# Performance work log

Measured on AMD Instinct MI355X. Metric: run time of the kernel, lower is better.

Reference implementation:

```python
import jax, jax.numpy as jnp
import numpy as np

J = 1.0
B, C, L = 16, 16, 128


def _masks(L):
    ii, jj = jnp.meshgrid(jnp.arange(L), jnp.arange(L), indexing='ij')
    black = ((ii + jj) % 2 == 0)
    return black, jnp.logical_not(black)


def _nbr_sum(s):
    # periodic up/down/left/right neighbor sum, same math as the (i±1)%L gathers
    return (jnp.roll(s, 1, -2) + jnp.roll(s, -1, -2)
            + jnp.roll(s, 1, -1) + jnp.roll(s, -1, -1))


def _half_update(spins, mask, T, key):
    # Metropolis on one checkerboard color: dE = 2*J*s*sum_nbrs
    dE = 2.0 * J * spins * _nbr_sum(spins)
    u = jax.random.uniform(key, spins.shape, dtype=spins.dtype)
    accept = u < jnp.exp(-dE / T[:, None, None, None])
    return jnp.where(jnp.logical_and(accept, mask), -spins, spins)


def _one_sweep(spins, T, key, black, white):
    k1, k2 = jax.random.split(key)
    spins = _half_update(spins, black, T, k1)
    return _half_update(spins, white, T, k2)


def _energy(spins):
    # E = -J * sum over bonds (right + down neighbors once each) -> [B, C]
    return -J * jnp.sum(spins * (jnp.roll(spins, -1, -2) + jnp.roll(spins, -1, -1)), axis=(-2, -1))


def _pt_exchange(spins, T, key):
    nB = T.shape[0]
    P = nB // 2
    E = _energy(spins)                       # [B, C]
    beta = 1.0 / T
    E0, E1 = E[0:2 * P:2], E[1:2 * P:2]
    d = (beta[0:2 * P:2] - beta[1:2 * P:2])[:, None] * (E0 - E1)  # [P, C]
    u = jax.random.uniform(key, d.shape, dtype=spins.dtype)
    # accept prob min(1, exp(d)); exp(min(d,0)) is overflow-safe and equivalent
    acc = (u < jnp.exp(jnp.minimum(d, 0.0)))[:, :, None, None]
    s0, s1 = spins[0:2 * P:2], spins[1:2 * P:2]
    spins = spins.at[0:2 * P:2].set(jnp.where(acc, s1, s0))
    spins = spins.at[1:2 * P:2].set(jnp.where(acc, s0, s1))
    return spins


def _simulate(spins_init, T, n_sweeps, n_therm, decorrelate, pt_interval):
    Lx = spins_init.shape[-1]
    black, white = _masks(Lx)
    base = jax.random.key(42)

    def step_fn(spins, i):
        k = jax.random.fold_in(base, i)
        spins = _one_sweep(spins, T, k, black, white)
        spins = jax.lax.cond(i % pt_interval == 0,
                             lambda s: _pt_exchange(s, T, jax.random.fold_in(k, 123)),
                             lambda s: s, spins)
        return spins, None

    # thermalization
    spins, _ = jax.lax.scan(step_fn, spins_init, jnp.arange(n_therm))

    # production: record one sample per decorrelate sweeps
    num_samples = n_sweeps // decorrelate

    def block_fn(spins, b):
        spins, _ = jax.lax.scan(lambda s, j: step_fn(s, n_therm + b * decorrelate + j),
                                spins, jnp.arange(decorrelate))
        return spins, spins

    spins, samples = jax.lax.scan(block_fn, spins, jnp.arange(num_samples))
    # samples: [S, B, C, L, L] -> [B, C*S, L, L]
    Bn, Cn = spins.shape[0], spins.shape[1]
    return jnp.transpose(samples, (1, 0, 2, 3, 4)).reshape(Bn, num_samples * Cn, Lx, Lx)


def setup_inputs() -> dict:
    key = jax.random.key(0)
    k1, _ = jax.random.split(key)
    x = jax.random.normal(k1, (B, C, L, L), dtype=jnp.float32)
    spins_init = jnp.where(x >= 0, 1.0, -1.0).astype(jnp.float32)  # ±1 Ising spins
    T = jnp.linspace(1.0, 3.5, B).astype(jnp.float32)              # temperature ladder
    return {"spins_init": spins_init, "T": T, "n_sweeps": 10, "n_therm": 10,
            "decorrelate": 5, "pt_interval": 5}


def reference(spins_init, T, n_sweeps, n_therm, decorrelate, pt_interval):
    return _simulate(spins_init, T, n_sweeps, n_therm, decorrelate, pt_interval)
```

## Files before the change

### kernel.cpp

```cpp
#include <hip/hip_runtime.h>
#include <stdint.h>


#define LSZ   128
#define NB    16
#define NC    16
#define NSITES (NB*NC*LSZ*LSZ)

__host__ __device__ __forceinline__ void tf2x32(uint32_t k0, uint32_t k1,
                                                uint32_t x0, uint32_t x1,
                                                uint32_t& o0, uint32_t& o1) {
  uint32_t k2 = k0 ^ k1 ^ 0x1BD11BDAu;
  x0 += k0; x1 += k1;
#define TFR(r) { x0 += x1; x1 = (x1 << (r)) | (x1 >> (32 - (r))); x1 ^= x0; }
  TFR(13) TFR(15) TFR(26) TFR(6)
  x0 += k1; x1 += k2 + 1u;
  TFR(17) TFR(29) TFR(16) TFR(24)
  x0 += k2; x1 += k0 + 2u;
  TFR(13) TFR(15) TFR(26) TFR(6)
  x0 += k0; x1 += k1 + 3u;
  TFR(17) TFR(29) TFR(16) TFR(24)
  x0 += k1; x1 += k2 + 4u;
  TFR(13) TFR(15) TFR(26) TFR(6)
  x0 += k2; x1 += k0 + 5u;
#undef TFR
  o0 = x0; o1 = x1;
}

__device__ __forceinline__ float tf_uniform(uint32_t w) {
  union { uint32_t u; float f; } cvt;
  cvt.u = (w >> 9) | 0x3f800000u;
  return cvt.f - 1.0f;
}

__device__ __forceinline__ int sb(uint32_t w, int b) {
  return (int)((int32_t)(w << ((3 - b) * 8)) >> 24);
}

__global__ __launch_bounds__(512) void k_chunk(const float4* __restrict__ in4,
                                               uint32_t* __restrict__ sg,
                                               const float* __restrict__ T,
                                               int* __restrict__ slotmap,
                                               const float* __restrict__ Eprev,
                                               float* __restrict__ Ecur,
                                               float* __restrict__ out,
                                               int chunk, int start, int nsw,
                                               int sample_local, int sidx,
                                               int write_E, int store_back) {
  __shared__ __align__(16) uint32_t lat32[LSZ * LSZ / 4];
  __shared__ uint32_t kb[5][4];
  __shared__ float sh_p4, sh_p8;
  __shared__ int sh_bp;
  __shared__ int wred[8];

  const int w = blockIdx.x;
  const int t = threadIdx.x;
  const int c = w & 15;

  if (t < nsw) {
    uint32_t kk0, kk1, a, b;
    tf2x32(0u, 42u, 0u, (uint32_t)(start + t), kk0, kk1);
    tf2x32(kk0, kk1, 0u, 0u, a, b);
    kb[t][0] = a; kb[t][1] = b;
    tf2x32(kk0, kk1, 0u, 1u, a, b);
    kb[t][2] = a; kb[t][3] = b;
  }

  if (chunk == 0) {
    for (int k = 0; k < 8; ++k) {
      int idx = k * 512 + t;
      float4 v = in4[(w << 12) + idx];
      lat32[idx] = (v.x >= 0.0f ? 0x01u : 0xFFu)
                 | ((v.y >= 0.0f ? 0x01u : 0xFFu) << 8)
                 | ((v.z >= 0.0f ? 0x01u : 0xFFu) << 16)
                 | ((v.w >= 0.0f ? 0x01u : 0xFFu) << 24);
    }
  } else {
    for (int k = 0; k < 2; ++k)
      ((uint4*)lat32)[k * 512 + t] = ((const uint4*)sg)[(w << 10) + k * 512 + t];
  }

  if (t == 0) {
    int bp;
    if (chunk == 0) {
      bp = w >> 4;
    } else {
      bp = slotmap[w];
      int p = bp >> 1;
      float E0 = Eprev[(2 * p) * NC + c];
      float E1 = Eprev[(2 * p + 1) * NC + c];
      float b0 = 1.0f / T[2 * p];
      float b1 = 1.0f / T[2 * p + 1];
      float d = (b0 - b1) * (E0 - E1);
      uint32_t kk0, kk1, p0, p1, w0, w1;
      tf2x32(0u, 42u, 0u, (uint32_t)(start - 1), kk0, kk1);
      tf2x32(kk0, kk1, 0u, 123u, p0, p1);
      tf2x32(p0, p1, 0u, (uint32_t)(p * NC + c), w0, w1);
      float u = tf_uniform(w0 ^ w1);
      float pa = (d < 0.0f) ? (float)exp((double)d) : 1.0f;
      if (u < pa) bp ^= 1;
    }
    slotmap[w] = bp;
    sh_bp = bp;
    float Tb = T[bp];
    sh_p4 = (float)exp((double)(-4.0f / Tb));
    sh_p8 = (float)exp((double)(-8.0f / Tb));
  }
  __syncthreads();

  const int bp = sh_bp;
  const float p4 = sh_p4, p8 = sh_p8;
  const int r    = t >> 2;
  const int sg32 = t & 3;
  const int col0 = sg32 << 5;
  const uint32_t rowbase = ((uint32_t)((bp << 4) | c) << 14) + ((uint32_t)r << 7);
  const int8_t* latb = (const int8_t*)lat32;
  const int own4 = (r << 3) + (sg32 << 1);

  for (int sw = 0; sw < nsw; ++sw) {
    for (int par = 0; par < 2; ++par) {
      const uint32_t kk0 = kb[sw][par * 2];
      const uint32_t kk1 = kb[sw][par * 2 + 1];
      const int j0 = (r + par) & 1;

      uint32_t cw[8], uw[8], dw[8];
      {
        uint4 a  = ((const uint4*)lat32)[own4];
        uint4 b2 = ((const uint4*)lat32)[own4 + 1];
        cw[0]=a.x; cw[1]=a.y; cw[2]=a.z; cw[3]=a.w;
        cw[4]=b2.x; cw[5]=b2.y; cw[6]=b2.z; cw[7]=b2.w;
        int u4 = (((r - 1) & 127) << 3) + (sg32 << 1);
        a  = ((const uint4*)lat32)[u4];
        b2 = ((const uint4*)lat32)[u4 + 1];
        uw[0]=a.x; uw[1]=a.y; uw[2]=a.z; uw[3]=a.w;
        uw[4]=b2.x; uw[5]=b2.y; uw[6]=b2.z; uw[7]=b2.w;
        int d4 = (((r + 1) & 127) << 3) + (sg32 << 1);
        a  = ((const uint4*)lat32)[d4];
        b2 = ((const uint4*)lat32)[d4 + 1];
        dw[0]=a.x; dw[1]=a.y; dw[2]=a.z; dw[3]=a.w;
        dw[4]=b2.x; dw[5]=b2.y; dw[6]=b2.z; dw[7]=b2.w;
      }
      int lfb = latb[(r << 7) + ((col0 - 1) & 127)];
      int rtb = latb[(r << 7) + ((col0 + 32) & 127)];

      uint32_t ex[9];
      ex[0] = (cw[0] << 8) | (uint32_t)(uint8_t)lfb;
#pragma unroll
      for (int i = 1; i < 8; ++i) ex[i] = (cw[i - 1] >> 24) | (cw[i] << 8);
      ex[8] = (cw[7] >> 24) | ((uint32_t)(uint8_t)rtb << 8);
      uint32_t Y[9], U[8], D[8];
#pragma unroll
      for (int i = 0; i < 8; ++i) {
        Y[i] = j0 ? ((ex[i] >> 8) | (ex[i + 1] << 24)) : ex[i];
        U[i] = j0 ? ((uw[i] >> 8) | ((i < 7 ? uw[i + 1] : 0u) << 24)) : uw[i];
        D[i] = j0 ? ((dw[i] >> 8) | ((i < 7 ? dw[i + 1] : 0u) << 24)) : dw[i];
      }
      Y[8] = j0 ? (ex[8] >> 8) : ex[8];

      const uint32_t mbase = 0xFEu << (8 * j0);
      uint32_t xm[8];
#pragma unroll
      for (int i = 0; i < 8; ++i) xm[i] = 0u;
      const uint32_t cnt0 = rowbase + (uint32_t)(col0 + j0);
#pragma unroll
      for (int m = 0; m < 16; ++m) {
        int lf = sb(Y[(2 * m) >> 2], (2 * m) & 3);
        int s0 = sb(Y[(2 * m + 1) >> 2], (2 * m + 1) & 3);
        int rt = sb(Y[(2 * m + 2) >> 2], (2 * m + 2) & 3);
        int up = sb(U[(2 * m) >> 2], (2 * m) & 3);
        int dn = sb(D[(2 * m) >> 2], (2 * m) & 3);
        int q = s0 * (lf + rt + up + dn);
        uint32_t o0, o1;
        tf2x32(kk0, kk1, 0u, cnt0 + 2u * (uint32_t)m, o0, o1);
        float u = tf_uniform(o0 ^ o1);
        bool a = (q <= 0) || (u < (q == 4 ? p8 : p4));
        if (a) xm[m >> 1] |= (m & 1) ? (mbase << 16) : mbase;
      }
      uint4 n0, n1;
      n0.x = cw[0] ^ xm[0]; n0.y = cw[1] ^ xm[1];
      n0.z = cw[2] ^ xm[2]; n0.w = cw[3] ^ xm[3];
      n1.x = cw[4] ^ xm[4]; n1.y = cw[5] ^ xm[5];
      n1.z = cw[6] ^ xm[6]; n1.w = cw[7] ^ xm[7];
      ((uint4*)lat32)[own4]     = n0;
      ((uint4*)lat32)[own4 + 1] = n1;
      __syncthreads();
    }

    if (sw == sample_local) {
      float4* dst = (float4*)out
                  + (((size_t)((bp << 5) + (sidx << 4) + c)) << 12)
                  + (r << 5) + (sg32 << 3);
      const uint32_t* own = lat32 + (r << 5) + (sg32 << 3);
#pragma unroll
      for (int qd = 0; qd < 8; ++qd) {
        uint32_t v = own[qd];
        float4 f;
        f.x = (float)sb(v, 0); f.y = (float)sb(v, 1);
        f.z = (float)sb(v, 2); f.w = (float)sb(v, 3);
        dst[qd] = f;
      }
    }
  }

  if (write_E) {
    uint32_t cw[8], dw[8];
    {
      uint4 a  = ((const uint4*)lat32)[own4];
      uint4 b2 = ((const uint4*)lat32)[own4 + 1];
      cw[0]=a.x; cw[1]=a.y; cw[2]=a.z; cw[3]=a.w;
      cw[4]=b2.x; cw[5]=b2.y; cw[6]=b2.z; cw[7]=b2.w;
      int d4 = (((r + 1) & 127) << 3) + (sg32 << 1);
      a  = ((const uint4*)lat32)[d4];
      b2 = ((const uint4*)lat32)[d4 + 1];
      dw[0]=a.x; dw[1]=a.y; dw[2]=a.z; dw[3]=a.w;
      dw[4]=b2.x; dw[5]=b2.y; dw[6]=b2.z; dw[7]=b2.w;
    }
    int rb = latb[(r << 7) + ((col0 + 32) & 127)];
    int psum = 0;
#pragma unroll
    for (int i = 0; i < 32; ++i) {
      int ci = sb(cw[i >> 2], i & 3);
      int di = sb(dw[i >> 2], i & 3);
      int ri = (i < 31) ? sb(cw[(i + 1) >> 2], (i + 1) & 3) : rb;
      psum += ci * (di + ri);
    }
#pragma unroll
    for (int o = 32; o > 0; o >>= 1) psum += __shfl_down(psum, o, 64);
    if ((t & 63) == 0) wred[t >> 6] = psum;
    __syncthreads();
    if (t == 0) {
      int tot = 0;
#pragma unroll
      for (int i = 0; i < 8; ++i) tot += wred[i];
      Ecur[(bp << 4) | c] = -(float)tot;
    }
  }

  if (store_back) {
    for (int k = 0; k < 2; ++k)
      ((uint4*)sg)[(w << 10) + k * 512 + t] = ((const uint4*)lat32)[k * 512 + t];
  }
}

extern "C" void kernel_launch(void* const* d_in, const int* in_sizes, int n_in,
                              void* d_out, int out_size, void* d_ws, size_t ws_size,
                              hipStream_t stream) {
  const float* spins_in = (const float*)d_in[0];
  const float* T        = (const float*)d_in[1];
  uint32_t* s   = (uint32_t*)d_ws;
  float*  Ea    = (float*)((char*)d_ws + (4u << 20));
  float*  Eb    = (float*)((char*)d_ws + (4u << 20) + 1024);
  int*  slotmap = (int*)((char*)d_ws + (4u << 20) + 2048);
  float*  out = (float*)d_out;

  const int starts[5]  = {0, 1, 6, 11, 16};
  const int counts[5]  = {1, 5, 5, 5, 4};
  const int samploc[5] = {-1, -1, -1, 3, 3};
  const int sampidx[5] = {0, 0, 0, 0, 1};
  const int writeE[5]  = {1, 1, 1, 1, 0};
  const int storeB[5]  = {1, 1, 1, 1, 0};

  for (int ch = 0; ch < 5; ++ch) {
    float* Ecur  = (ch & 1) ? Eb : Ea;
    float* Eprev = (ch & 1) ? Ea : Eb;
    k_chunk<<<256, 512, 0, stream>>>((const float4*)spins_in, s, T, slotmap,
                                     Eprev, Ecur, out,
                                     ch, starts[ch], counts[ch],
                                     samploc[ch], sampidx[ch],
                                     writeE[ch], storeB[ch]);
  }
}
```

Baseline: 290.6 us.

## Double threads per lattice, pair Threefry streams, and use integer acceptance thresholds

Each 128x128 lattice block now runs 1024 threads instead of 512, so each thread handles 16 columns instead of 32. With 256 blocks on a device with 256 CUs, this doubles the per-CU parallelism that hides latency in the RNG-heavy Metropolis loop. Two Threefry evaluations are interleaved in one function to raise ILP, and the float uniform compare is replaced by comparing the top 23 random bits against precomputed integer thresholds. The risks are higher register pressure under 1024-thread launch bounds, and a possible off-by-rounding mismatch between the ceil-based threshold and the float compare.

```diff
diff --git a/kernel.cpp b/kernel.cpp
--- a/kernel.cpp
+++ b/kernel.cpp
@@ -27,6 +27,31 @@
   o0 = x0; o1 = x1;
 }
 
+__device__ __forceinline__ void tf2x32x2(uint32_t k0, uint32_t k1,
+                                         uint32_t xa, uint32_t xb,
+                                         uint32_t& oa, uint32_t& ob) {
+  uint32_t k2 = k0 ^ k1 ^ 0x1BD11BDAu;
+  uint32_t a0 = k0, a1 = xa + k1;
+  uint32_t b0 = k0, b1 = xb + k1;
+#define TFR2(r) { a0 += a1; b0 += b1; \
+                  a1 = __builtin_rotateleft32(a1, r); \
+                  b1 = __builtin_rotateleft32(b1, r); \
+                  a1 ^= a0; b1 ^= b0; }
+  TFR2(13) TFR2(15) TFR2(26) TFR2(6)
+  a0 += k1; a1 += k2 + 1u; b0 += k1; b1 += k2 + 1u;
+  TFR2(17) TFR2(29) TFR2(16) TFR2(24)
+  a0 += k2; a1 += k0 + 2u; b0 += k2; b1 += k0 + 2u;
+  TFR2(13) TFR2(15) TFR2(26) TFR2(6)
+  a0 += k0; a1 += k1 + 3u; b0 += k0; b1 += k1 + 3u;
+  TFR2(17) TFR2(29) TFR2(16) TFR2(24)
+  a0 += k1; a1 += k2 + 4u; b0 += k1; b1 += k2 + 4u;
+  TFR2(13) TFR2(15) TFR2(26) TFR2(6)
+  a0 += k2; a1 += k0 + 5u; b0 += k2; b1 += k0 + 5u;
+#undef TFR2
+  oa = a0 ^ a1;
+  ob = b0 ^ b1;
+}
+
 __device__ __forceinline__ float tf_uniform(uint32_t w) {
   union { uint32_t u; float f; } cvt;
   cvt.u = (w >> 9) | 0x3f800000u;
@@ -37,21 +62,21 @@
   return (int)((int32_t)(w << ((3 - b) * 8)) >> 24);
 }
 
-__global__ __launch_bounds__(512) void k_chunk(const float4* __restrict__ in4,
-                                               uint32_t* __restrict__ sg,
-                                               const float* __restrict__ T,
-                                               int* __restrict__ slotmap,
-                                               const float* __restrict__ Eprev,
-                                               float* __restrict__ Ecur,
-                                               float* __restrict__ out,
-                                               int chunk, int start, int nsw,
-                                               int sample_local, int sidx,
-                                               int write_E, int store_back) {
+__global__ __launch_bounds__(1024) void k_chunk(const float4* __restrict__ in4,
+                                                uint32_t* __restrict__ sg,
+                                                const float* __restrict__ T,
+                                                int* __restrict__ slotmap,
+                                                const float* __restrict__ Eprev,
+                                                float* __restrict__ Ecur,
+                                                float* __restrict__ out,
+                                                int chunk, int start, int nsw,
+                                                int sample_local, int sidx,
+                                                int write_E, int store_back) {
   __shared__ __align__(16) uint32_t lat32[LSZ * LSZ / 4];
   __shared__ uint32_t kb[5][4];
-  __shared__ float sh_p4, sh_p8;
+  __shared__ uint32_t sh_T4, sh_T8;
   __shared__ int sh_bp;
-  __shared__ int wred[8];
+  __shared__ int wred[16];
 
   const int w = blockIdx.x;
   const int t = threadIdx.x;
@@ -67,8 +92,8 @@
   }
 
   if (chunk == 0) {
-    for (int k = 0; k < 8; ++k) {
-      int idx = k * 512 + t;
+    for (int k = 0; k < 4; ++k) {
+      int idx = k * 1024 + t;
       float4 v = in4[(w << 12) + idx];
       lat32[idx] = (v.x >= 0.0f ? 0x01u : 0xFFu)
                  | ((v.y >= 0.0f ? 0x01u : 0xFFu) << 8)
@@ -76,8 +101,7 @@
                  | ((v.w >= 0.0f ? 0x01u : 0xFFu) << 24);
     }
   } else {
-    for (int k = 0; k < 2; ++k)
-      ((uint4*)lat32)[k * 512 + t] = ((const uint4*)sg)[(w << 10) + k * 512 + t];
+    ((uint4*)lat32)[t] = ((const uint4*)sg)[(w << 10) + t];
   }
 
   if (t == 0) {
@@ -103,19 +127,22 @@
     slotmap[w] = bp;
     sh_bp = bp;
     float Tb = T[bp];
-    sh_p4 = (float)exp((double)(-4.0f / Tb));
-    sh_p8 = (float)exp((double)(-8.0f / Tb));
+    float p4 = (float)exp((double)(-4.0f / Tb));
+    float p8 = (float)exp((double)(-8.0f / Tb));
+    sh_T4 = (uint32_t)ceil((double)p4 * 8388608.0);
+    sh_T8 = (uint32_t)ceil((double)p8 * 8388608.0);
   }
   __syncthreads();
 
   const int bp = sh_bp;
-  const float p4 = sh_p4, p8 = sh_p8;
-  const int r    = t >> 2;
-  const int sg32 = t & 3;
-  const int col0 = sg32 << 5;
+  const uint32_t T4 = sh_T4, T8 = sh_T8;
+  const uint32_t TOPEN = 0x00800000u;
+  const int r    = t >> 3;
+  const int seg  = t & 7;
+  const int col0 = seg << 4;
   const uint32_t rowbase = ((uint32_t)((bp << 4) | c) << 14) + ((uint32_t)r << 7);
   const int8_t* latb = (const int8_t*)lat32;
-  const int own4 = (r << 3) + (sg32 << 1);
+  const int own4 = (r << 3) + seg;
 
   for (int sw = 0; sw < nsw; ++sw) {
     for (int par = 0; par < 2; ++par) {
@@ -123,105 +150,95 @@
       const uint32_t kk1 = kb[sw][par * 2 + 1];
       const int j0 = (r + par) & 1;
 
-      uint32_t cw[8], uw[8], dw[8];
-      {
-        uint4 a  = ((const uint4*)lat32)[own4];
-        uint4 b2 = ((const uint4*)lat32)[own4 + 1];
-        cw[0]=a.x; cw[1]=a.y; cw[2]=a.z; cw[3]=a.w;
-        cw[4]=b2.x; cw[5]=b2.y; cw[6]=b2.z; cw[7]=b2.w;
-        int u4 = (((r - 1) & 127) << 3) + (sg32 << 1);
-        a  = ((const uint4*)lat32)[u4];
-        b2 = ((const uint4*)lat32)[u4 + 1];
-        uw[0]=a.x; uw[1]=a.y; uw[2]=a.z; uw[3]=a.w;
-        uw[4]=b2.x; uw[5]=b2.y; uw[6]=b2.z; uw[7]=b2.w;
-        int d4 = (((r + 1) & 127) << 3) + (sg32 << 1);
-        a  = ((const uint4*)lat32)[d4];
-        b2 = ((const uint4*)lat32)[d4 + 1];
-        dw[0]=a.x; dw[1]=a.y; dw[2]=a.z; dw[3]=a.w;
-        dw[4]=b2.x; dw[5]=b2.y; dw[6]=b2.z; dw[7]=b2.w;
+      uint4 cv = ((const uint4*)lat32)[own4];
+      uint4 uv = ((const uint4*)lat32)[(((r - 1) & 127) << 3) + seg];
+      uint4 dv = ((const uint4*)lat32)[(((r + 1) & 127) << 3) + seg];
+      int lfb = latb[(r << 7) + ((col0 - 1) & 127)];
+      int rtb = latb[(r << 7) + ((col0 + 16) & 127)];
+
+      uint32_t cw[4] = {cv.x, cv.y, cv.z, cv.w};
+      uint32_t uw[4] = {uv.x, uv.y, uv.z, uv.w};
+      uint32_t dw[4] = {dv.x, dv.y, dv.z, dv.w};
+
+      uint32_t ext[5];
+      ext[0] = (cw[0] << 8) | (uint32_t)(uint8_t)lfb;
+      ext[1] = (cw[0] >> 24) | (cw[1] << 8);
+      ext[2] = (cw[1] >> 24) | (cw[2] << 8);
+      ext[3] = (cw[2] >> 24) | (cw[3] << 8);
+      ext[4] = (cw[3] >> 24) | ((uint32_t)(uint8_t)rtb << 8);
+      uint32_t Y[5], U[4], D[4];
+#pragma unroll
+      for (int i = 0; i < 4; ++i) {
+        uint32_t sh = (ext[i] >> 8) | (ext[i + 1] << 24);
+        Y[i] = j0 ? sh : ext[i];
+        uint32_t su = (uw[i] >> 8) | ((i < 3 ? uw[i + 1] : 0u) << 24);
+        U[i] = j0 ? su : uw[i];
+        uint32_t sd = (dw[i] >> 8) | ((i < 3 ? dw[i + 1] : 0u) << 24);
+        D[i] = j0 ? sd : dw[i];
       }
-      int lfb = latb[(r << 7) + ((col0 - 1) & 127)];
-      int rtb = latb[(r << 7) + ((col0 + 32) & 127)];
-
-      uint32_t ex[9];
-      ex[0] = (cw[0] << 8) | (uint32_t)(uint8_t)lfb;
-#pragma unroll
-      for (int i = 1; i < 8; ++i) ex[i] = (cw[i - 1] >> 24) | (cw[i] << 8);
-      ex[8] = (cw[7] >> 24) | ((uint32_t)(uint8_t)rtb << 8);
-      uint32_t Y[9], U[8], D[8];
-#pragma unroll
-      for (int i = 0; i < 8; ++i) {
-        Y[i] = j0 ? ((ex[i] >> 8) | (ex[i + 1] << 24)) : ex[i];
-        U[i] = j0 ? ((uw[i] >> 8) | ((i < 7 ? uw[i + 1] : 0u) << 24)) : uw[i];
-        D[i] = j0 ? ((dw[i] >> 8) | ((i < 7 ? dw[i + 1] : 0u) << 24)) : dw[i];
+      Y[4] = j0 ? (ext[4] >> 8) : ext[4];
+
+      const uint32_t mbase = 0xFEu << (8 * j0);
+      uint32_t xm[4] = {0u, 0u, 0u, 0u};
+      const uint32_t cnt0 = rowbase + (uint32_t)(col0 + j0);
+#pragma unroll
+      for (int m2 = 0; m2 < 4; ++m2) {
+        const int ma = 2 * m2, mb = 2 * m2 + 1;
+        int lfa = sb(Y[(2 * ma) >> 2], (2 * ma) & 3);
+        int s0a = sb(Y[(2 * ma + 1) >> 2], (2 * ma + 1) & 3);
+        int rta = sb(Y[(2 * ma + 2) >> 2], (2 * ma + 2) & 3);
+        int upa = sb(U[(2 * ma) >> 2], (2 * ma) & 3);
+        int dna = sb(D[(2 * ma) >> 2], (2 * ma) & 3);
+        int qa = s0a * (lfa + rta + upa + dna);
+        int lfb2 = sb(Y[(2 * mb) >> 2], (2 * mb) & 3);
+        int s0b = sb(Y[(2 * mb + 1) >> 2], (2 * mb + 1) & 3);
+        int rtb2 = sb(Y[(2 * mb + 2) >> 2], (2 * mb + 2) & 3);
+        int upb = sb(U[(2 * mb) >> 2], (2 * mb) & 3);
+        int dnb = sb(D[(2 * mb) >> 2], (2 * mb) & 3);
+        int qb = s0b * (lfb2 + rtb2 + upb + dnb);
+        uint32_t wa, wb;
+        tf2x32x2(kk0, kk1, cnt0 + 2u * (uint32_t)ma, cnt0 + 2u * (uint32_t)mb,
+                 wa, wb);
+        uint32_t ta = (qa <= 0) ? TOPEN : (qa == 4 ? T8 : T4);
+        uint32_t tb = (qb <= 0) ? TOPEN : (qb == 4 ? T8 : T4);
+        if ((wa >> 9) < ta) xm[m2] |= mbase;
+        if ((wb >> 9) < tb) xm[m2] |= (mbase << 16);
       }
-      Y[8] = j0 ? (ex[8] >> 8) : ex[8];
-
-      const uint32_t mbase = 0xFEu << (8 * j0);
-      uint32_t xm[8];
-#pragma unroll
-      for (int i = 0; i < 8; ++i) xm[i] = 0u;
-      const uint32_t cnt0 = rowbase + (uint32_t)(col0 + j0);
-#pragma unroll
-      for (int m = 0; m < 16; ++m) {
-        int lf = sb(Y[(2 * m) >> 2], (2 * m) & 3);
-        int s0 = sb(Y[(2 * m + 1) >> 2], (2 * m + 1) & 3);
-        int rt = sb(Y[(2 * m + 2) >> 2], (2 * m + 2) & 3);
-        int up = sb(U[(2 * m) >> 2], (2 * m) & 3);
-        int dn = sb(D[(2 * m) >> 2], (2 * m) & 3);
-        int q = s0 * (lf + rt + up + dn);
-        uint32_t o0, o1;
-        tf2x32(kk0, kk1, 0u, cnt0 + 2u * (uint32_t)m, o0, o1);
-        float u = tf_uniform(o0 ^ o1);
-        bool a = (q <= 0) || (u < (q == 4 ? p8 : p4));
-        if (a) xm[m >> 1] |= (m & 1) ? (mbase << 16) : mbase;
-      }
-      uint4 n0, n1;
-      n0.x = cw[0] ^ xm[0]; n0.y = cw[1] ^ xm[1];
-      n0.z = cw[2] ^ xm[2]; n0.w = cw[3] ^ xm[3];
-      n1.x = cw[4] ^ xm[4]; n1.y = cw[5] ^ xm[5];
-      n1.z = cw[6] ^ xm[6]; n1.w = cw[7] ^ xm[7];
-      ((uint4*)lat32)[own4]     = n0;
-      ((uint4*)lat32)[own4 + 1] = n1;
+      uint4 nv;
+      nv.x = cw[0] ^ xm[0]; nv.y = cw[1] ^ xm[1];
+      nv.z = cw[2] ^ xm[2]; nv.w = cw[3] ^ xm[3];
+      ((uint4*)lat32)[own4] = nv;
       __syncthreads();
     }
 
     if (sw == sample_local) {
+      uint4 cv = ((const uint4*)lat32)[own4];
       float4* dst = (float4*)out
                   + (((size_t)((bp << 5) + (sidx << 4) + c)) << 12)
-                  + (r << 5) + (sg32 << 3);
-      const uint32_t* own = lat32 + (r << 5) + (sg32 << 3);
-#pragma unroll
-      for (int qd = 0; qd < 8; ++qd) {
-        uint32_t v = own[qd];
+                  + (r << 5) + (seg << 2);
+      uint32_t wv[4] = {cv.x, cv.y, cv.z, cv.w};
+#pragma unroll
+      for (int qd = 0; qd < 4; ++qd) {
         float4 f;
-        f.x = (float)sb(v, 0); f.y = (float)sb(v, 1);
-        f.z = (float)sb(v, 2); f.w = (float)sb(v, 3);
+        f.x = (float)sb(wv[qd], 0); f.y = (float)sb(wv[qd], 1);
+        f.z = (float)sb(wv[qd], 2); f.w = (float)sb(wv[qd], 3);
         dst[qd] = f;
       }
     }
   }
 
   if (write_E) {
-    uint32_t cw[8], dw[8];
-    {
-      uint4 a  = ((const uint4*)lat32)[own4];
-      uint4 b2 = ((const uint4*)lat32)[own4 + 1];
-      cw[0]=a.x; cw[1]=a.y; cw[2]=a.z; cw[3]=a.w;
-      cw[4]=b2.x; cw[5]=b2.y; cw[6]=b2.z; cw[7]=b2.w;
-      int d4 = (((r + 1) & 127) << 3) + (sg32 << 1);
-      a  = ((const uint4*)lat32)[d4];
-      b2 = ((const uint4*)lat32)[d4 + 1];
-      dw[0]=a.x; dw[1]=a.y; dw[2]=a.z; dw[3]=a.w;
-      dw[4]=b2.x; dw[5]=b2.y; dw[6]=b2.z; dw[7]=b2.w;
-    }
-    int rb = latb[(r << 7) + ((col0 + 32) & 127)];
+    uint4 cv = ((const uint4*)lat32)[own4];
+    uint4 dv = ((const uint4*)lat32)[(((r + 1) & 127) << 3) + seg];
+    int rb = latb[(r << 7) + ((col0 + 16) & 127)];
+    uint32_t cw[4] = {cv.x, cv.y, cv.z, cv.w};
+    uint32_t dw[4] = {dv.x, dv.y, dv.z, dv.w};
     int psum = 0;
 #pragma unroll
-    for (int i = 0; i < 32; ++i) {
+    for (int i = 0; i < 16; ++i) {
       int ci = sb(cw[i >> 2], i & 3);
       int di = sb(dw[i >> 2], i & 3);
-      int ri = (i < 31) ? sb(cw[(i + 1) >> 2], (i + 1) & 3) : rb;
+      int ri = (i < 15) ? sb(cw[(i + 1) >> 2], (i + 1) & 3) : rb;
       psum += ci * (di + ri);
     }
 #pragma unroll
@@ -231,14 +248,13 @@
     if (t == 0) {
       int tot = 0;
 #pragma unroll
-      for (int i = 0; i < 8; ++i) tot += wred[i];
+      for (int i = 0; i < 16; ++i) tot += wred[i];
       Ecur[(bp << 4) | c] = -(float)tot;
     }
   }
 
   if (store_back) {
-    for (int k = 0; k < 2; ++k)
-      ((uint4*)sg)[(w << 10) + k * 512 + t] = ((const uint4*)lat32)[k * 512 + t];
+    ((uint4*)sg)[(w << 10) + t] = ((const uint4*)lat32)[t];
   }
 }
 
@@ -263,10 +279,10 @@
   for (int ch = 0; ch < 5; ++ch) {
     float* Ecur  = (ch & 1) ? Eb : Ea;
     float* Eprev = (ch & 1) ? Ea : Eb;
-    k_chunk<<<256, 512, 0, stream>>>((const float4*)spins_in, s, T, slotmap,
-                                     Eprev, Ecur, out,
-                                     ch, starts[ch], counts[ch],
-                                     samploc[ch], sampidx[ch],
-                                     writeE[ch], storeB[ch]);
-  }
-}
+    k_chunk<<<256, 1024, 0, stream>>>((const float4*)spins_in, s, T, slotmap,
+                                      Eprev, Ecur, out,
+                                      ch, starts[ch], counts[ch],
+                                      samploc[ch], sampidx[ch],
+                                      writeE[ch], storeB[ch]);
+  }
+}
```

Result: faster. 283.5 us (-2.4%).
